# Optimization experiments

Measured on AMD Instinct MI355X. Metric: run time of the kernel, lower is better.

## Reference

```python
import jax, jax.numpy as jnp
import numpy as np

N = 200_000      # nodes
E = 6_400_000    # edges (avg degree 32)
ATT = 16         # scorer hidden dim
MAXD = 512       # mixer max_depth
C = 1.0          # curvature
EPS = 1e-15


def _mobius_add(a, b, c):
    # Mobius addition on the Poincare ball: a (+)_c b
    ab = jnp.sum(a * b, axis=-1, keepdims=True)
    aa = jnp.sum(a * a, axis=-1, keepdims=True)
    bb = jnp.sum(b * b, axis=-1, keepdims=True)
    num = (1.0 + 2.0 * c * ab + c * bb) * a + (1.0 - c * aa) * b
    den = 1.0 + 2.0 * c * ab + (c * c) * aa * bb
    return num / jnp.maximum(den, EPS)


def setup_inputs() -> dict:
    key = jax.random.key(0)
    ks = jax.random.split(key, 8)
    x = jax.random.normal(ks[0], (N, 2), dtype=jnp.float32)
    # keep nodes strictly inside the unit Poincare disk (|x| < 0.5)
    x = 0.5 * x / (1.0 + jnp.linalg.norm(x, axis=-1, keepdims=True))
    edge_index = jax.random.randint(ks[1], (2, E), 0, N, dtype=jnp.int32)
    depth = jax.random.randint(ks[2], (N,), 0, MAXD, dtype=jnp.int32)
    W1 = jax.random.normal(ks[3], (2, ATT), dtype=jnp.float32) * (1.0 / np.sqrt(2.0))
    b1 = jnp.zeros((ATT,), dtype=jnp.float32)
    W2 = jax.random.normal(ks[4], (ATT, 1), dtype=jnp.float32) * (1.0 / np.sqrt(ATT))
    eta = jnp.array(1.0, dtype=jnp.float32)
    depth_scale = 1.0 + 0.1 * jax.random.normal(ks[5], (MAXD, 1), dtype=jnp.float32)
    depth_theta = 0.1 * jax.random.normal(ks[6], (MAXD, 1), dtype=jnp.float32)
    return dict(x=x, edge_index=edge_index, depth=depth, W1=W1, b1=b1, W2=W2,
                eta=eta, depth_scale=depth_scale, depth_theta=depth_theta)


def reference(x, edge_index, depth, W1, b1, W2, eta, depth_scale, depth_theta):
    c = C
    sc = jnp.sqrt(jnp.asarray(c, dtype=x.dtype))
    row, col = edge_index[0], edge_index[1]
    xi = x[row]   # [E,2] target node of each edge
    xj = x[col]   # [E,2] source node of each edge

    # log_{xi}(xj): tangent vector at xi
    u = _mobius_add(-xi, xj, c)                                        # [E,2]
    un = jnp.maximum(jnp.linalg.norm(u, axis=-1, keepdims=True), EPS)  # [E,1]
    lam_i = 2.0 / jnp.maximum(1.0 - c * jnp.sum(xi * xi, axis=-1, keepdims=True), EPS)
    v = (2.0 / (sc * lam_i)) * jnp.arctanh(jnp.minimum(sc * un, 1.0 - 1e-5)) * (u / un)

    # tiny MLP attention score per edge
    h = jax.nn.gelu(v @ W1 + b1, approximate=False)   # [E,ATT]
    scores = (h @ W2)[:, 0]                           # [E]

    # segment softmax over edges grouped by target node `row`
    smax = jax.ops.segment_max(scores, row, num_segments=N)
    ex = jnp.exp(scores - smax[row])
    denom = jax.ops.segment_sum(ex, row, num_segments=N)
    alpha = ex / jnp.maximum(denom[row], 1e-15)       # [E]

    # weighted scatter-add of tangent vectors
    m = jax.ops.segment_sum(alpha[:, None] * v, row, num_segments=N)   # [N,2]

    # depth-gated rotation/scale in the tangent space (mixer)
    d = jnp.clip(depth, 0, MAXD - 1)
    k = depth_scale[d]            # [N,1]
    ang = depth_theta[d][:, 0]    # [N]
    ca, sa = jnp.cos(ang), jnp.sin(ang)
    m = k * jnp.stack([ca * m[:, 0] - sa * m[:, 1],
                       sa * m[:, 0] + ca * m[:, 1]], axis=-1)

    # exp_{x}(eta * m)
    w = eta * m
    wn = jnp.maximum(jnp.linalg.norm(w, axis=-1, keepdims=True), EPS)
    lam_x = 2.0 / jnp.maximum(1.0 - c * jnp.sum(x * x, axis=-1, keepdims=True), EPS)
    second = jnp.tanh(sc * lam_x * wn / 2.0) * (w / (sc * wn))
    return _mobius_add(x, second, c)
```

## Files before the change

kernel.cpp:

```cpp
#include <hip/hip_runtime.h>
#include <hip/hip_fp16.h>
#include <math.h>

#define EPSF 1e-15f
#define BSH  8
#define BSZ  (1 << BSH)
#define BMSK (BSZ - 1)
#define CAPB 9216
#define MAXNB 1024
#define AGG_T 1024
#define KSL   9
#define BIN_T 1024
#define LCH   4096

#define TBL   128
#define TW    129
#define TWSZ  (TW * TW)
#define VMIN  (-1.2f)
#define VH    (2.4f / 128.0f)
#define INVH  (128.0f / 2.4f)

__device__ __forceinline__ float fast_rcp(float x)  { return __builtin_amdgcn_rcpf(x); }
__device__ __forceinline__ float fast_rsq(float x)  { return __builtin_amdgcn_rsqf(x); }
__device__ __forceinline__ float fast_exp(float x)  { return __builtin_amdgcn_exp2f(x * 1.4426950408889634f); }

__device__ __forceinline__ unsigned int float_to_ordered(float f) {
    unsigned int u = __float_as_uint(f);
    return (u & 0x80000000u) ? ~u : (u | 0x80000000u);
}
__device__ __forceinline__ float ordered_to_float(unsigned int u) {
    u = (u & 0x80000000u) ? (u & 0x7FFFFFFFu) : ~u;
    return __uint_as_float(u);
}

__device__ __forceinline__ void edge_v_fast(float2 xi, float2 xj, float& vx, float& vy) {
    float ab = -(xi.x * xj.x + xi.y * xj.y);
    float aa = xi.x * xi.x + xi.y * xi.y;
    float bb = xj.x * xj.x + xj.y * xj.y;
    float f1 = 1.0f + 2.0f * ab + bb;
    float f2 = 1.0f - aa;
    float ux = f1 * (-xi.x) + f2 * xj.x;
    float uy = f1 * (-xi.y) + f2 * xj.y;
    float den = 1.0f + 2.0f * ab + aa * bb;
    float inv_den = fast_rcp(fmaxf(den, EPSF));
    ux *= inv_den; uy *= inv_den;
    float un2 = fmaxf(ux * ux + uy * uy, 1e-24f);
    float inv_un = fast_rsq(un2);
    float un = fminf(un2 * inv_un, 1.0f - 1e-5f);
    float t = 0.34657359027997264f * __builtin_amdgcn_logf((1.0f + un) * fast_rcp(1.0f - un));
    float s = fmaxf(f2, EPSF) * t * inv_un;
    vx = s * ux; vy = s * uy;
}

__device__ __forceinline__ void edge_v(float2 xi, float2 xj, float& vx, float& vy) {
    float ab = -(xi.x * xj.x + xi.y * xj.y);
    float aa = xi.x * xi.x + xi.y * xi.y;
    float bb = xj.x * xj.x + xj.y * xj.y;
    float f1 = 1.0f + 2.0f * ab + bb;
    float f2 = 1.0f - aa;
    float ux = f1 * (-xi.x) + f2 * xj.x;
    float uy = f1 * (-xi.y) + f2 * xj.y;
    float den = 1.0f + 2.0f * ab + aa * bb;
    float inv_den = 1.0f / fmaxf(den, EPSF);
    ux *= inv_den; uy *= inv_den;
    float un = fmaxf(sqrtf(ux * ux + uy * uy), EPSF);
    float t  = atanhf(fminf(un, 1.0f - 1e-5f));
    float s = fmaxf(f2, EPSF) * t / un;
    vx = s * ux; vy = s * uy;
}

__device__ __forceinline__ float edge_score(float vx, float vy,
                                            const float* __restrict__ W1,
                                            const float* __restrict__ b1,
                                            const float* __restrict__ W2) {
    float score = 0.0f;
#pragma unroll
    for (int k = 0; k < 16; ++k) {
        float z = fmaf(vx, W1[k], fmaf(vy, W1[16 + k], b1[k]));
        float g = 0.5f * z * (1.0f + erff(z * 0.70710678118654752f));
        score = fmaf(g, W2[k], score);
    }
    return score;
}

__device__ __forceinline__ float2 finalize_node(float2 xv, float mx, float my,
                                                int d, float eta,
                                                const float* __restrict__ dscale,
                                                const float* __restrict__ dtheta) {
    d = d < 0 ? 0 : (d > 511 ? 511 : d);
    float k   = dscale[d];
    float ang = dtheta[d];
    float ca = cosf(ang), sa = sinf(ang);
    float m0 = k * (ca * mx - sa * my);
    float m1 = k * (sa * mx + ca * my);

    float wx = eta * m0, wy = eta * m1;
    float wn = fmaxf(sqrtf(wx * wx + wy * wy), 1e-15f);

    float aa = xv.x * xv.x + xv.y * xv.y;
    float lam = 2.0f / fmaxf(1.0f - aa, 1e-15f);
    float fac = tanhf(lam * wn * 0.5f) / wn;
    float sx = fac * wx, sy = fac * wy;

    float ab = xv.x * sx + xv.y * sy;
    float bb = sx * sx + sy * sy;
    float n1 = 1.0f + 2.0f * ab + bb;
    float n2 = 1.0f - aa;
    float ox = n1 * xv.x + n2 * sx;
    float oy = n1 * xv.y + n2 * sy;
    float dd = 1.0f + 2.0f * ab + aa * bb;
    float inv = 1.0f / fmaxf(dd, 1e-15f);
    return make_float2(ox * inv, oy * inv);
}


__global__ void init_cursor(unsigned* __restrict__ cursor, int NB) {
    int b = blockIdx.x * blockDim.x + threadIdx.x;
    if (b < NB) cursor[b] = (unsigned)b * CAPB;
}

__global__ void build_score_table(const float* __restrict__ W1,
                                  const float* __restrict__ b1,
                                  const float* __restrict__ W2,
                                  float* __restrict__ tbl) {
    int i = blockIdx.x * blockDim.x + threadIdx.x;
    if (i >= TWSZ) return;
    int iy = i / TW, ix = i - iy * TW;
    float vx = VMIN + VH * (float)ix;
    float vy = VMIN + VH * (float)iy;
    tbl[i] = edge_score(vx, vy, W1, b1, W2);
}

__global__ __launch_bounds__(BIN_T, 8)
void bin_edges(const int* __restrict__ ei,
               unsigned* __restrict__ cursor,
               unsigned* __restrict__ sorted,
               int E, int NB) {
    __shared__ unsigned bkrank[LCH];
    __shared__ unsigned payload[LCH];
    __shared__ unsigned sortedLoc[LCH];
    __shared__ unsigned gdst[LCH];
    __shared__ unsigned hist[MAXNB];
    __shared__ unsigned loc[MAXNB];
    __shared__ unsigned gbase[MAXNB];
    __shared__ unsigned waveSum[16];

    int tid = threadIdx.x;
    int e0 = blockIdx.x * LCH;
    int cnt = min(E - e0, LCH);
    if (cnt <= 0) return;

    hist[tid] = 0;
    __syncthreads();

    for (int idx = tid; idx < cnt; idx += BIN_T) {
        int r = ei[e0 + idx];
        int c = ei[E + e0 + idx];
        unsigned bk = (unsigned)r >> BSH;
        unsigned rank = atomicAdd(&hist[bk], 1u);
        bkrank[idx] = (bk << 14) | rank;
        payload[idx] = ((unsigned)(r & BMSK) << 24) | (unsigned)c;
    }
    __syncthreads();

    unsigned h = hist[tid];
    unsigned v = h;
    int lane = tid & 63;
    int wv = tid >> 6;
#pragma unroll
    for (int s = 1; s < 64; s <<= 1) {
        unsigned t = __shfl_up(v, s, 64);
        if (lane >= s) v += t;
    }
    if (lane == 63) waveSum[wv] = v;
    __syncthreads();
    if (wv == 0) {
        unsigned w2 = (lane < 16) ? waveSum[lane] : 0u;
#pragma unroll
        for (int s = 1; s < 16; s <<= 1) {
            unsigned t = __shfl_up(w2, s, 64);
            if (lane >= s) w2 += t;
        }
        if (lane < 16) waveSum[lane] = w2;
    }
    __syncthreads();
    unsigned base = wv ? waveSum[wv - 1] : 0u;
    loc[tid] = base + v - h;
    gbase[tid] = h ? atomicAdd(&cursor[tid], h) : 0u;
    __syncthreads();

    for (int idx = tid; idx < cnt; idx += BIN_T) {
        unsigned w = bkrank[idx];
        unsigned bk = w >> 14;
        unsigned rank = w & 0x3FFFu;
        unsigned pos = loc[bk] + rank;
        sortedLoc[pos] = payload[idx];
        unsigned g = gbase[bk] + rank;
        gdst[pos] = (g < (bk + 1u) * CAPB) ? g : 0xFFFFFFFFu;
    }
    __syncthreads();

    for (int idx = tid; idx < cnt; idx += BIN_T) {
        unsigned g = gdst[idx];
        if (g != 0xFFFFFFFFu) sorted[g] = sortedLoc[idx];
    }
}

__global__ __launch_bounds__(AGG_T, 8)
void aggregate(const float2* __restrict__ x,
               const unsigned* __restrict__ cursor,
               const unsigned* __restrict__ sorted,
               const int* __restrict__ depth,
               const float* __restrict__ tbl,
               const float* __restrict__ etaPtr,
               const float* __restrict__ dscale,
               const float* __restrict__ dtheta,
               float2* __restrict__ out, int N) {
    __shared__ float tl[TWSZ];
    __shared__ float2 xr[BSZ];
    __shared__ unsigned nmax[BSZ];
    __shared__ unsigned long long accP[BSZ];

    int b = blockIdx.x;
    int tid = threadIdx.x;
    int nb0 = b << BSH;
    int nodeCnt = min(BSZ, N - nb0);

    unsigned basep = (unsigned)b * CAPB;
    const unsigned* __restrict__ sb = sorted + basep;

    unsigned u[KSL];
#pragma unroll
    for (int k = 0; k < KSL; ++k) {
        u[k] = sb[(unsigned)tid + (unsigned)(k * AGG_T)];
    }
    __builtin_amdgcn_sched_barrier(0);

    for (int i = tid; i < TWSZ; i += AGG_T) tl[i] = tbl[i];
    if (tid < BSZ) {
        nmax[tid] = 0u;
        accP[tid] = 0ull;
        if (tid < nodeCnt) xr[tid] = x[nb0 + tid];
    }

    unsigned cnt = cursor[b] - basep;
    cnt = cnt > (unsigned)CAPB ? (unsigned)CAPB : cnt;

    float2 xj[KSL];
#pragma unroll
    for (int k = 0; k < KSL; ++k) {
        unsigned i = (unsigned)tid + (unsigned)(k * AGG_T);
        int c = (i < cnt) ? (int)(u[k] & 0xFFFFFFu) : 0;
        xj[k] = x[c];
    }
    __builtin_amdgcn_sched_barrier(0);
    __syncthreads();

    unsigned pkA[KSL];
    unsigned pkV[KSL];
#pragma unroll
    for (int k = 0; k < KSL; ++k) {
        unsigned i = (unsigned)tid + (unsigned)(k * AGG_T);
        bool act = i < cnt;
        int rl = (int)(u[k] >> 24);
        float2 xi = xr[rl];
        float vx, vy;
        edge_v_fast(xi, xj[k], vx, vy);

        float tx = fminf(fmaxf((vx - VMIN) * INVH, 0.0f), 127.999f);
        float ty = fminf(fmaxf((vy - VMIN) * INVH, 0.0f), 127.999f);
        int ix = (int)tx, iy = (int)ty;
        float fx = tx - (float)ix, fy = ty - (float)iy;
        const float* row = tl + iy * TW + ix;
        float s00 = row[0], s01 = row[1];
        float s10 = row[TW], s11 = row[TW + 1];
        float sA = fmaf(fx, s01 - s00, s00);
        float sB = fmaf(fx, s11 - s10, s10);
        float score = fmaf(fy, sB - sA, sA);

        __half hs = __float2half_rn(score);
        float sq = __half2float(hs);
        unsigned short s16 = *(unsigned short*)&hs;
        __half2 h2 = __floats2half2_rn(vx, vy);
        pkA[k] = ((unsigned)rl << 16) | (unsigned)s16;
        pkV[k] = *(unsigned*)&h2;
        if (act) atomicMax(&nmax[rl], float_to_ordered(sq));
    }
    __syncthreads();

#pragma unroll
    for (int k = 0; k < KSL; ++k) {
        unsigned i = (unsigned)tid + (unsigned)(k * AGG_T);
        if (i >= cnt) continue;
        int rlk = (int)(pkA[k] >> 16);
        unsigned short s16 = (unsigned short)(pkA[k] & 0xFFFFu);
        __half hs = *(__half*)&s16;
        float s = __half2float(hs);
        float mxs = ordered_to_float(nmax[rlk]);
        float ex = fast_exp(s - mxs);
        __half2 h2 = *(__half2*)&pkV[k];
        float2 v2 = __half22float2(h2);
        unsigned e0 = __float2uint_rn(ex * 16384.0f);
        unsigned e1 = __float2uint_rn(ex * (v2.x + 2.0f) * 0.25f * 16384.0f);
        unsigned e2 = __float2uint_rn(ex * (v2.y + 2.0f) * 0.25f * 16384.0f);
        unsigned long long pk = (unsigned long long)e0
                              | ((unsigned long long)e1 << 21)
                              | ((unsigned long long)e2 << 42);
        atomicAdd(&accP[rlk], pk);
    }
    __syncthreads();

    if (tid >= nodeCnt) return;
    unsigned long long w = accP[tid];
    float F0 = (float)(unsigned int)(w & 0x1FFFFFull);
    float F1 = (float)(unsigned int)((w >> 21) & 0x1FFFFFull);
    float F2 = (float)(unsigned int)(w >> 42);
    float mx = 0.0f, my = 0.0f;
    if (F0 > 0.0f) {
        float inv = 1.0f / F0;
        mx = 4.0f * F1 * inv - 2.0f;
        my = 4.0f * F2 * inv - 2.0f;
    }
    int i = nb0 + tid;
    out[i] = finalize_node(xr[tid], mx, my, depth[i], etaPtr[0], dscale, dtheta);
}


__global__ void init_kernel(unsigned int* __restrict__ smax,
                            unsigned long long* __restrict__ maccP, int N) {
    int i = blockIdx.x * blockDim.x + threadIdx.x;
    if (i < N) {
        smax[i] = float_to_ordered(-INFINITY);
        maccP[i] = 0ull;
    }
}

__global__ void pass1_score_max(const float2* __restrict__ x,
                                const int* __restrict__ ei,
                                const float* __restrict__ W1,
                                const float* __restrict__ b1,
                                const float* __restrict__ W2,
                                unsigned int* __restrict__ smax, int E) {
    int e = blockIdx.x * blockDim.x + threadIdx.x;
    if (e >= E) return;
    int r = ei[e];
    int c = ei[E + e];
    float vx, vy;
    edge_v(x[r], x[c], vx, vy);
    float score = edge_score(vx, vy, W1, b1, W2);
    atomicMax(&smax[r], float_to_ordered(score));
}

#define PK_SCALE 16384.0f

__global__ void pass2_accum(const float2* __restrict__ x,
                            const int* __restrict__ ei,
                            const float* __restrict__ W1,
                            const float* __restrict__ b1,
                            const float* __restrict__ W2,
                            const unsigned int* __restrict__ smax,
                            unsigned long long* __restrict__ maccP, int E) {
    int e = blockIdx.x * blockDim.x + threadIdx.x;
    if (e >= E) return;
    int r = ei[e];
    int c = ei[E + e];
    float vx, vy;
    edge_v(x[r], x[c], vx, vy);
    float score = edge_score(vx, vy, W1, b1, W2);
    float mx = ordered_to_float(smax[r]);
    float ex = expf(score - mx);
    unsigned e0 = __float2uint_rn(ex * PK_SCALE);
    unsigned e1 = __float2uint_rn(ex * (vx + 2.0f) * 0.25f * PK_SCALE);
    unsigned e2 = __float2uint_rn(ex * (vy + 2.0f) * 0.25f * PK_SCALE);
    unsigned long long pk = (unsigned long long)e0
                          | ((unsigned long long)e1 << 21)
                          | ((unsigned long long)e2 << 42);
    atomicAdd(&maccP[r], pk);
}

__global__ void pass3_finalize(const float2* __restrict__ x,
                               const int* __restrict__ depth,
                               const unsigned long long* __restrict__ maccP,
                               const float* __restrict__ etaPtr,
                               const float* __restrict__ dscale,
                               const float* __restrict__ dtheta,
                               float2* __restrict__ out, int N) {
    int i = blockIdx.x * blockDim.x + threadIdx.x;
    if (i >= N) return;
    unsigned long long w = maccP[i];
    float F0 = (float)(unsigned int)(w & 0x1FFFFFull);
    float F1 = (float)(unsigned int)((w >> 21) & 0x1FFFFFull);
    float F2 = (float)(unsigned int)(w >> 42);
    float mx = 0.0f, my = 0.0f;
    if (F0 > 0.0f) {
        float inv = 1.0f / F0;
        mx = 4.0f * F1 * inv - 2.0f;
        my = 4.0f * F2 * inv - 2.0f;
    }
    out[i] = finalize_node(x[i], mx, my, depth[i], etaPtr[0], dscale, dtheta);
}


extern "C" void kernel_launch(void* const* d_in, const int* in_sizes, int n_in,
                              void* d_out, int out_size, void* d_ws, size_t ws_size,
                              hipStream_t stream) {
    const float2* x   = (const float2*)d_in[0];
    const int* ei     = (const int*)d_in[1];
    const int* depth  = (const int*)d_in[2];
    const float* W1   = (const float*)d_in[3];
    const float* b1   = (const float*)d_in[4];
    const float* W2   = (const float*)d_in[5];
    const float* eta  = (const float*)d_in[6];
    const float* dsc  = (const float*)d_in[7];
    const float* dth  = (const float*)d_in[8];
    float2* out = (float2*)d_out;

    int N = in_sizes[0] / 2;
    int E = in_sizes[1] / 2;
    int NB = (N + BSZ - 1) >> BSH;

    const int B = 256;
    size_t sortedBytes = (size_t)NB * CAPB * 4;
    size_t need = 4096 + sortedBytes + (size_t)TWSZ * 4;
    if (NB <= MAXNB && ws_size >= need) {
        unsigned* cursor = (unsigned*)d_ws;
        unsigned* sorted = (unsigned*)((char*)d_ws + 4096);
        float* tbl = (float*)((char*)d_ws + 4096 + sortedBytes);
        int binG = (E + LCH - 1) / LCH;
        init_cursor<<<(NB + B - 1) / B, B, 0, stream>>>(cursor, NB);
        build_score_table<<<(TWSZ + B - 1) / B, B, 0, stream>>>(W1, b1, W2, tbl);
        bin_edges<<<binG, BIN_T, 0, stream>>>(ei, cursor, sorted, E, NB);
        aggregate<<<NB, AGG_T, 0, stream>>>(x, cursor, sorted, depth, tbl,
                                            eta, dsc, dth, out, N);
    } else {
        unsigned long long* maccP = (unsigned long long*)d_ws;
        unsigned int* smax = (unsigned int*)(maccP + N);
        init_kernel<<<(N + B - 1) / B, B, 0, stream>>>(smax, maccP, N);
        pass1_score_max<<<(E + B - 1) / B, B, 0, stream>>>(x, ei, W1, b1, W2, smax, E);
        pass2_accum<<<(E + B - 1) / B, B, 0, stream>>>(x, ei, W1, b1, W2, smax, maccP, E);
        pass3_finalize<<<(N + B - 1) / B, B, 0, stream>>>(x, depth, maccP, eta, dsc, dth, out, N);
    }
}
```

Before: 186.6 us.

## Fuse score-table build into binning, vectorize edge loads, memset cursors

Score-table construction moves into the bin_edges kernel when there are enough blocks, and a memset replaces the init_cursor kernel. Together these cut two launches down to one memset. Bin_edges now loads edge indices as int4 when E and the chunk size are multiples of 4. The scatter stores a local rank and computes the global address later, and cursors become relative counts. Aggregate reads its bucket with uint4 loads and remaps slot indices to match, which changes the lane-to-edge mapping and the atomic contention pattern.

```diff
diff --git a/kernel.cpp b/kernel.cpp
--- a/kernel.cpp
+++ b/kernel.cpp
@@ -114,11 +114,6 @@
 }
 
 
-__global__ void init_cursor(unsigned* __restrict__ cursor, int NB) {
-    int b = blockIdx.x * blockDim.x + threadIdx.x;
-    if (b < NB) cursor[b] = (unsigned)b * CAPB;
-}
-
 __global__ void build_score_table(const float* __restrict__ W1,
                                   const float* __restrict__ b1,
                                   const float* __restrict__ W2,
@@ -135,9 +130,13 @@
 void bin_edges(const int* __restrict__ ei,
                unsigned* __restrict__ cursor,
                unsigned* __restrict__ sorted,
-               int E, int NB) {
-    __shared__ unsigned bkrank[LCH];
-    __shared__ unsigned payload[LCH];
+               int E, int NB, int buildTbl,
+               const float* __restrict__ W1,
+               const float* __restrict__ b1,
+               const float* __restrict__ W2,
+               float* __restrict__ tbl) {
+    __shared__ __align__(16) unsigned bkrank[LCH];
+    __shared__ __align__(16) unsigned payload[LCH];
     __shared__ unsigned sortedLoc[LCH];
     __shared__ unsigned gdst[LCH];
     __shared__ unsigned hist[MAXNB];
@@ -146,6 +145,17 @@
     __shared__ unsigned waveSum[16];
 
     int tid = threadIdx.x;
+
+    if (buildTbl) {
+        int gi = blockIdx.x * BIN_T + tid;
+        if (gi < TWSZ) {
+            int iy = gi / TW, ix = gi - iy * TW;
+            float vx = VMIN + VH * (float)ix;
+            float vy = VMIN + VH * (float)iy;
+            tbl[gi] = edge_score(vx, vy, W1, b1, W2);
+        }
+    }
+
     int e0 = blockIdx.x * LCH;
     int cnt = min(E - e0, LCH);
     if (cnt <= 0) return;
@@ -153,13 +163,33 @@
     hist[tid] = 0;
     __syncthreads();
 
-    for (int idx = tid; idx < cnt; idx += BIN_T) {
-        int r = ei[e0 + idx];
-        int c = ei[E + e0 + idx];
-        unsigned bk = (unsigned)r >> BSH;
-        unsigned rank = atomicAdd(&hist[bk], 1u);
-        bkrank[idx] = (bk << 14) | rank;
-        payload[idx] = ((unsigned)(r & BMSK) << 24) | (unsigned)c;
+    if (((E | cnt) & 3) == 0) {
+        int idx = tid << 2;
+        if (idx < cnt) {
+            const int4 r4 = *(const int4*)(ei + e0 + idx);
+            const int4 c4 = *(const int4*)(ei + E + e0 + idx);
+            unsigned bk0 = (unsigned)r4.x >> BSH; unsigned rk0 = atomicAdd(&hist[bk0], 1u);
+            unsigned bk1 = (unsigned)r4.y >> BSH; unsigned rk1 = atomicAdd(&hist[bk1], 1u);
+            unsigned bk2 = (unsigned)r4.z >> BSH; unsigned rk2 = atomicAdd(&hist[bk2], 1u);
+            unsigned bk3 = (unsigned)r4.w >> BSH; unsigned rk3 = atomicAdd(&hist[bk3], 1u);
+            *(uint4*)(bkrank + idx) = make_uint4((bk0 << 14) | rk0, (bk1 << 14) | rk1,
+                                                 (bk2 << 14) | rk2, (bk3 << 14) | rk3);
+            uint4 pl;
+            pl.x = ((unsigned)(r4.x & BMSK) << 24) | (unsigned)c4.x;
+            pl.y = ((unsigned)(r4.y & BMSK) << 24) | (unsigned)c4.y;
+            pl.z = ((unsigned)(r4.z & BMSK) << 24) | (unsigned)c4.z;
+            pl.w = ((unsigned)(r4.w & BMSK) << 24) | (unsigned)c4.w;
+            *(uint4*)(payload + idx) = pl;
+        }
+    } else {
+        for (int idx = tid; idx < cnt; idx += BIN_T) {
+            int r = ei[e0 + idx];
+            int c = ei[E + e0 + idx];
+            unsigned bk = (unsigned)r >> BSH;
+            unsigned rank = atomicAdd(&hist[bk], 1u);
+            bkrank[idx] = (bk << 14) | rank;
+            payload[idx] = ((unsigned)(r & BMSK) << 24) | (unsigned)c;
+        }
     }
     __syncthreads();
 
@@ -186,23 +216,23 @@
     __syncthreads();
     unsigned base = wv ? waveSum[wv - 1] : 0u;
     loc[tid] = base + v - h;
+
     gbase[tid] = h ? atomicAdd(&cursor[tid], h) : 0u;
     __syncthreads();
 
     for (int idx = tid; idx < cnt; idx += BIN_T) {
         unsigned w = bkrank[idx];
+        unsigned pos = loc[w >> 14] + (w & 0x3FFFu);
+        sortedLoc[pos] = payload[idx];
+        gdst[pos] = w;
+    }
+    __syncthreads();
+
+    for (int idx = tid; idx < cnt; idx += BIN_T) {
+        unsigned w = gdst[idx];
         unsigned bk = w >> 14;
-        unsigned rank = w & 0x3FFFu;
-        unsigned pos = loc[bk] + rank;
-        sortedLoc[pos] = payload[idx];
-        unsigned g = gbase[bk] + rank;
-        gdst[pos] = (g < (bk + 1u) * CAPB) ? g : 0xFFFFFFFFu;
-    }
-    __syncthreads();
-
-    for (int idx = tid; idx < cnt; idx += BIN_T) {
-        unsigned g = gdst[idx];
-        if (g != 0xFFFFFFFFu) sorted[g] = sortedLoc[idx];
+        unsigned rel = gbase[bk] + (w & 0x3FFFu);
+        if (rel < (unsigned)CAPB) sorted[bk * (unsigned)CAPB + rel] = sortedLoc[idx];
     }
 }
 
@@ -226,13 +256,16 @@
     int nb0 = b << BSH;
     int nodeCnt = min(BSZ, N - nb0);
 
-    unsigned basep = (unsigned)b * CAPB;
-    const unsigned* __restrict__ sb = sorted + basep;
+    const unsigned* __restrict__ sb = sorted + (unsigned)b * CAPB;
 
     unsigned u[KSL];
-#pragma unroll
-    for (int k = 0; k < KSL; ++k) {
-        u[k] = sb[(unsigned)tid + (unsigned)(k * AGG_T)];
+    {
+        uint4 ua = *(const uint4*)(sb + 4 * tid);
+        uint4 ub = *(const uint4*)(sb + 4096 + 4 * tid);
+        unsigned uc = sb[8192 + tid];
+        u[0] = ua.x; u[1] = ua.y; u[2] = ua.z; u[3] = ua.w;
+        u[4] = ub.x; u[5] = ub.y; u[6] = ub.z; u[7] = ub.w;
+        u[8] = uc;
     }
     __builtin_amdgcn_sched_barrier(0);
 
@@ -243,13 +276,17 @@
         if (tid < nodeCnt) xr[tid] = x[nb0 + tid];
     }
 
-    unsigned cnt = cursor[b] - basep;
+    unsigned cnt = cursor[b];
     cnt = cnt > (unsigned)CAPB ? (unsigned)CAPB : cnt;
 
+#define SLOT(k) ((k) < 4 ? (unsigned)(4 * tid + (k)) \
+               : (k) < 8 ? (unsigned)(4096 + 4 * tid + ((k) - 4)) \
+                         : (unsigned)(8192 + tid))
+
     float2 xj[KSL];
 #pragma unroll
     for (int k = 0; k < KSL; ++k) {
-        unsigned i = (unsigned)tid + (unsigned)(k * AGG_T);
+        unsigned i = SLOT(k);
         int c = (i < cnt) ? (int)(u[k] & 0xFFFFFFu) : 0;
         xj[k] = x[c];
     }
@@ -260,7 +297,7 @@
     unsigned pkV[KSL];
 #pragma unroll
     for (int k = 0; k < KSL; ++k) {
-        unsigned i = (unsigned)tid + (unsigned)(k * AGG_T);
+        unsigned i = SLOT(k);
         bool act = i < cnt;
         int rl = (int)(u[k] >> 24);
         float2 xi = xr[rl];
@@ -290,7 +327,7 @@
 
 #pragma unroll
     for (int k = 0; k < KSL; ++k) {
-        unsigned i = (unsigned)tid + (unsigned)(k * AGG_T);
+        unsigned i = SLOT(k);
         if (i >= cnt) continue;
         int rlk = (int)(pkA[k] >> 16);
         unsigned short s16 = (unsigned short)(pkA[k] & 0xFFFFu);
@@ -308,6 +345,7 @@
                               | ((unsigned long long)e2 << 42);
         atomicAdd(&accP[rlk], pk);
     }
+#undef SLOT
     __syncthreads();
 
     if (tid >= nodeCnt) return;
@@ -427,9 +465,13 @@
         unsigned* sorted = (unsigned*)((char*)d_ws + 4096);
         float* tbl = (float*)((char*)d_ws + 4096 + sortedBytes);
         int binG = (E + LCH - 1) / LCH;
-        init_cursor<<<(NB + B - 1) / B, B, 0, stream>>>(cursor, NB);
-        build_score_table<<<(TWSZ + B - 1) / B, B, 0, stream>>>(W1, b1, W2, tbl);
-        bin_edges<<<binG, BIN_T, 0, stream>>>(ei, cursor, sorted, E, NB);
+        int tblBlocks = (TWSZ + BIN_T - 1) / BIN_T;
+        int buildInBin = (binG >= tblBlocks) ? 1 : 0;
+        hipMemsetAsync(cursor, 0, (size_t)NB * sizeof(unsigned), stream);
+        if (!buildInBin)
+            build_score_table<<<(TWSZ + B - 1) / B, B, 0, stream>>>(W1, b1, W2, tbl);
+        bin_edges<<<binG, BIN_T, 0, stream>>>(ei, cursor, sorted, E, NB, buildInBin,
+                                              W1, b1, W2, tbl);
         aggregate<<<NB, AGG_T, 0, stream>>>(x, cursor, sorted, depth, tbl,
                                             eta, dsc, dth, out, N);
     } else {
```

Result: faster. 180.7 us (-3.1%).
